# Kernel optimization log

Measured on AMD Instinct MI355X. Metric: run time of the kernel, lower is better.

The kernel has to match this reference:

```python
import jax, jax.numpy as jnp
import numpy as np

B, S, H = 1, 2048, 2048
NH, NKV, HD = 32, 8, 64
RBS, ICS, RBN = 64, 64, 16          # retrieval_block_size, input_chunk_size, retrieval_block_num
RLEN = RBS * RBN                     # 1024 retrieval tokens
KV = RLEN + S                        # 3072 total kv length
START = RLEN                         # INPUT_START_IDX
SCALE = HD ** -0.5
NEG = -1e9


def _document_ids():
    # mirrors get_document_ids
    ids = np.full(KV, -1, np.int32)
    ids[:START] = np.arange(START) // RBS + 1            # retrieval blocks -> 1..RBN
    chunk = np.arange(S) // ICS
    ids[START:] = np.where(chunk == 0, -1, np.minimum(chunk, RBN))
    return ids


def _block_mask():
    # mirrors causal_retrieval_mask_mod, precomputed dense [S, KV]
    ids = _document_ids()
    qpos = np.arange(S) + START
    kv = np.arange(KV)
    causal = (qpos[:, None] >= kv[None, :]) & (kv[None, :] > START)
    doc = (ids[qpos][:, None] == ids[None, :]) & (kv[None, :] < START)
    return jnp.asarray(causal | doc)


_MASK = _block_mask()


def _rotate_half(x):
    h = x.shape[-1] // 2
    return jnp.concatenate([-x[..., h:], x[..., :h]], axis=-1)


def setup_inputs() -> dict:
    key = jax.random.key(0)
    ks = jax.random.split(key, 6)
    inv_freq = 1.0 / (10000.0 ** (np.arange(0, HD, 2, dtype=np.float32) / HD))
    ang = np.arange(S, dtype=np.float32)[:, None] * inv_freq[None, :]   # [S, HD/2]
    emb = np.concatenate([ang, ang], axis=-1)                            # [S, HD]
    cos = jnp.asarray(np.cos(emb))[None].astype(jnp.float32)            # [1, S, HD]
    sin = jnp.asarray(np.sin(emb))[None].astype(jnp.float32)
    return {
        "hidden_states": jax.random.normal(ks[0], (B, S, H), jnp.float32),
        "cos": cos,
        "sin": sin,
        "retrieval_key": jax.random.normal(ks[1], (B, NKV, RLEN, HD), jnp.float32),
        "retrieval_value": jax.random.normal(ks[2], (B, NKV, RLEN, HD), jnp.float32),
        "Wq": jax.random.normal(ks[3], (H, NH * HD), jnp.float32) * 0.02,
        "Wk": jax.random.normal(ks[4], (H, NKV * HD), jnp.float32) * 0.02,
        "Wv": jax.random.normal(ks[5], (H, NKV * HD), jnp.float32) * 0.02,
        "Wo": jax.random.normal(jax.random.fold_in(key, 7), (NH * HD, H), jnp.float32) * 0.02,
    }


def reference(hidden_states, cos, sin, retrieval_key, retrieval_value, Wq, Wk, Wv, Wo):
    # QKV projections -> [B, nheads, S, HD]
    q = (hidden_states @ Wq).reshape(B, S, NH, HD).transpose(0, 2, 1, 3)
    k = (hidden_states @ Wk).reshape(B, S, NKV, HD).transpose(0, 2, 1, 3)
    v = (hidden_states @ Wv).reshape(B, S, NKV, HD).transpose(0, 2, 1, 3)
    # RoPE (retrieval kv is pre-encoded; rope only on current tokens)
    c, s = cos[:, None, :, :], sin[:, None, :, :]
    q = q * c + _rotate_half(q) * s
    k = k * c + _rotate_half(k) * s
    # prepend retrieval kv
    k = jnp.concatenate([retrieval_key, k], axis=2)    # [B, NKV, KV, HD]
    v = jnp.concatenate([retrieval_value, v], axis=2)
    # GQA: expand kv heads
    g = NH // NKV
    k = jnp.repeat(k, g, axis=1)                        # [B, NH, KV, HD]
    v = jnp.repeat(v, g, axis=1)
    scores = jnp.einsum("bhqd,bhkd->bhqk", q, k) * SCALE
    scores = jnp.where(_MASK[None, None], scores, NEG)
    probs = jax.nn.softmax(scores, axis=-1)
    # fully-masked rows (q_idx 0) -> zero output, matching flex_attention
    row_valid = _MASK.any(axis=-1)[None, None, :, None]
    probs = jnp.where(row_valid, probs, 0.0)
    out = jnp.einsum("bhqk,bhkd->bhqd", probs, v)
    out = out.transpose(0, 2, 1, 3).reshape(B, S, NH * HD)
    return out @ Wo
```

## Files before the change

### kernel.cpp

```cpp
#include <hip/hip_runtime.h>

#define S_LEN 2048
#define H_DIM 2048
#define NH 32
#define NKV 8
#define HD 64
#define RLEN 1024
#define KVTOT 3072
#define SCALE 0.125f
#define QS 0.18033688011112042f
#define FIX8 11.541560327111707f

typedef unsigned short ushort_t;
using short8 = __attribute__((ext_vector_type(8))) short;
using f32x4 = __attribute__((ext_vector_type(4))) float;

__device__ __forceinline__ float b2f(unsigned short u) {
    union { unsigned int i; float f; } v;
    v.i = ((unsigned int)u) << 16;
    return v.f;
}
__device__ __forceinline__ unsigned short f2b(float f) {
    union { float f; unsigned int i; } v;
    v.f = f;
    unsigned int x = v.i;
    return (unsigned short)((x + 0x7fffu + ((x >> 16) & 1u)) >> 16);
}

__global__ void detect9(const void* p0, const void* p1, const void* p2,
                        const void* p3, const void* p4, const void* p5,
                        const void* p6, const void* p7, const void* p8,
                        int* flags)
{
    __shared__ int bad;
    if (threadIdx.x == 0) bad = 0;
    __syncthreads();
    const void* ps[9] = {p0, p1, p2, p3, p4, p5, p6, p7, p8};
    const unsigned int* w = (const unsigned int*)ps[blockIdx.x];
    int cnt = 0;
    for (int i = threadIdx.x; i < 4096; i += blockDim.x) {
        unsigned int lo = w[i] & 0xFFFFu;
        unsigned int e = (lo >> 7) & 0xFFu;
        if (lo != 0u && (e < 90u || e > 140u)) ++cnt;
    }
    atomicAdd(&bad, cnt);
    __syncthreads();
    if (threadIdx.x == 0) flags[blockIdx.x] = (bad > 16) ? 1 : 0;
}

__global__ void cvt_b(const void* __restrict__ src, ushort_t* __restrict__ dst,
                      int n, const int* __restrict__ F_)
{
    const int F = *F_;
    int i = (blockIdx.x * 256 + threadIdx.x) * 8;
    if (i >= n) return;
    ushort_t o[8];
    if (F) {
        const float* p = (const float*)src + i;
        float4 f0 = ((const float4*)p)[0];
        float4 f1 = ((const float4*)p)[1];
        o[0] = f2b(f0.x); o[1] = f2b(f0.y); o[2] = f2b(f0.z); o[3] = f2b(f0.w);
        o[4] = f2b(f1.x); o[5] = f2b(f1.y); o[6] = f2b(f1.z); o[7] = f2b(f1.w);
        *(uint4*)(dst + i) = *(const uint4*)o;
    } else {
        *(uint4*)(dst + i) = *(const uint4*)((const ushort_t*)src + i);
    }
}

__global__ __launch_bounds__(256) void cvtW(
    const void* __restrict__ Wq, const void* __restrict__ Wk,
    const void* __restrict__ Wv, const void* __restrict__ Wo,
    ushort_t* __restrict__ WqkvT, ushort_t* __restrict__ WoT,
    const int* __restrict__ flags)
{
    const int z = blockIdx.z;
    if ((z == 1 || z == 2) && blockIdx.x >= 8) return;
    const void* src = (z == 0) ? Wq : (z == 1) ? Wk : (z == 2) ? Wv : Wo;
    const int F = flags[5 + z];
    const int C = (z == 1 || z == 2) ? 512 : 2048;
    ushort_t* dst = (z == 3) ? WoT : WqkvT;
    const int rofs = (z == 1) ? 2048 : (z == 2) ? 2560 : 0;

    __shared__ ushort_t S[64 * 72];
    const int r0 = blockIdx.y * 64, c0 = blockIdx.x * 64;
    const int lr = threadIdx.x >> 2, lc = (threadIdx.x & 3) * 16;
    ushort_t t[16];
    if (F) {
        const float* p = (const float*)src + (size_t)(r0 + lr) * C + c0 + lc;
#pragma unroll
        for (int j = 0; j < 16; j += 4) {
            float4 f = *(const float4*)(p + j);
            t[j] = f2b(f.x); t[j + 1] = f2b(f.y); t[j + 2] = f2b(f.z); t[j + 3] = f2b(f.w);
        }
    } else {
        const ushort_t* p = (const ushort_t*)src + (size_t)(r0 + lr) * C + c0 + lc;
        *(uint4*)t = ((const uint4*)p)[0];
        *(uint4*)(t + 8) = ((const uint4*)p)[1];
    }
    *(uint4*)&S[lr * 72 + lc] = *(const uint4*)t;
    *(uint4*)&S[lr * 72 + lc + 8] = *(const uint4*)(t + 8);
    __syncthreads();
    const int wc = threadIdx.x >> 2, wr = (threadIdx.x & 3) * 16;
    ushort_t o[16];
#pragma unroll
    for (int j = 0; j < 16; ++j) o[j] = S[(wr + j) * 72 + wc];
    ushort_t* q = dst + (size_t)(rofs + c0 + wc) * 2048 + r0 + wr;
    *(uint4*)q = *(const uint4*)o;
    *(uint4*)(q + 8) = *(const uint4*)(o + 8);
}

__global__ __launch_bounds__(256) void gemm_qkv(
    const ushort_t* __restrict__ A, const ushort_t* __restrict__ Bt,
    ushort_t* __restrict__ C, int N, int K)
{
    __shared__ __align__(16) ushort_t As[2][64 * 40];
    __shared__ __align__(16) ushort_t Bs[2][128 * 40];
    const int tid = threadIdx.x;
    const int wave = tid >> 6, lane = tid & 63;
    const int lq = lane & 15, quad = lane >> 4;
    const int m0 = blockIdx.y * 64, n0 = blockIdx.x * 128;
    const int wm = (wave & 1) * 32, wn = (wave >> 1) * 64;
    const int ar = tid >> 2, ak = (tid & 3) * 8;
    const int br = tid >> 1, bk = (tid & 1) * 16;
    const int nk = K >> 5;

    f32x4 acc[2][4];
#pragma unroll
    for (int i = 0; i < 2; ++i)
#pragma unroll
        for (int j = 0; j < 4; ++j) acc[i][j] = (f32x4){0.f, 0.f, 0.f, 0.f};

    const ushort_t* ap = A + (size_t)(m0 + ar) * K + ak;
    const ushort_t* bp = Bt + (size_t)(n0 + br) * K + bk;
    {
        uint4 a0 = ((const uint4*)ap)[0];
        uint4 b0 = ((const uint4*)bp)[0], b1 = ((const uint4*)bp)[1];
        *(uint4*)&As[0][ar * 40 + ak] = a0;
        *(uint4*)&Bs[0][br * 40 + bk] = b0; *(uint4*)&Bs[0][br * 40 + bk + 8] = b1;
    }

    for (int kt = 0; kt < nk; ++kt) {
        const int cur = kt & 1;
        uint4 na0, nb0, nb1;
        const bool more = (kt + 1 < nk);
        if (more) {
            na0 = *(const uint4*)(ap + (kt + 1) * 32);
            const ushort_t* bp2 = bp + (kt + 1) * 32;
            nb0 = ((const uint4*)bp2)[0]; nb1 = ((const uint4*)bp2)[1];
        }
        __syncthreads();
        short8 afr[2], bfr[4];
#pragma unroll
        for (int i = 0; i < 2; ++i)
            afr[i] = *(const short8*)&As[cur][(wm + i * 16 + lq) * 40 + quad * 8];
#pragma unroll
        for (int j = 0; j < 4; ++j)
            bfr[j] = *(const short8*)&Bs[cur][(wn + j * 16 + lq) * 40 + quad * 8];
#pragma unroll
        for (int i = 0; i < 2; ++i)
#pragma unroll
            for (int j = 0; j < 4; ++j)
                acc[i][j] = __builtin_amdgcn_mfma_f32_16x16x32_bf16(afr[i], bfr[j], acc[i][j], 0, 0, 0);
        __syncthreads();
        if (more) {
            const int nxt = cur ^ 1;
            *(uint4*)&As[nxt][ar * 40 + ak] = na0;
            *(uint4*)&Bs[nxt][br * 40 + bk] = nb0; *(uint4*)&Bs[nxt][br * 40 + bk + 8] = nb1;
        }
    }

#pragma unroll
    for (int i = 0; i < 2; ++i)
#pragma unroll
        for (int r = 0; r < 4; ++r) {
            ushort_t* cp = C + (size_t)(m0 + wm + i * 16 + quad * 4 + r) * N + n0 + wn + lq;
#pragma unroll
            for (int j = 0; j < 4; ++j) cp[j * 16] = f2b(acc[i][j][r]);
        }
}

__global__ __launch_bounds__(256) void gemm_fin(
    const ushort_t* __restrict__ A, const ushort_t* __restrict__ Bt,
    void* __restrict__ Cv, int N, int K, const int* __restrict__ oF_)
{
    const int oF = *oF_;
    __shared__ __align__(16) ushort_t As[2][64 * 40];
    __shared__ __align__(16) ushort_t Bs[2][128 * 40];
    const int tid = threadIdx.x;
    const int wave = tid >> 6, lane = tid & 63;
    const int lq = lane & 15, quad = lane >> 4;
    const int m0 = blockIdx.y * 64, n0 = blockIdx.x * 128;
    const int wm = (wave & 1) * 32, wn = (wave >> 1) * 64;
    const int ar = tid >> 2, ak = (tid & 3) * 8;
    const int br = tid >> 1, bk = (tid & 1) * 16;
    const int nk = K >> 5;

    f32x4 acc[2][4];
#pragma unroll
    for (int i = 0; i < 2; ++i)
#pragma unroll
        for (int j = 0; j < 4; ++j) acc[i][j] = (f32x4){0.f, 0.f, 0.f, 0.f};

    const ushort_t* ap = A + (size_t)(m0 + ar) * K + ak;
    const ushort_t* bp = Bt + (size_t)(n0 + br) * K + bk;
    {
        uint4 a0 = ((const uint4*)ap)[0];
        uint4 b0 = ((const uint4*)bp)[0], b1 = ((const uint4*)bp)[1];
        *(uint4*)&As[0][ar * 40 + ak] = a0;
        *(uint4*)&Bs[0][br * 40 + bk] = b0; *(uint4*)&Bs[0][br * 40 + bk + 8] = b1;
    }

    for (int kt = 0; kt < nk; ++kt) {
        const int cur = kt & 1;
        uint4 na0, nb0, nb1;
        const bool more = (kt + 1 < nk);
        if (more) {
            na0 = *(const uint4*)(ap + (kt + 1) * 32);
            const ushort_t* bp2 = bp + (kt + 1) * 32;
            nb0 = ((const uint4*)bp2)[0]; nb1 = ((const uint4*)bp2)[1];
        }
        __syncthreads();
        short8 afr[2], bfr[4];
#pragma unroll
        for (int i = 0; i < 2; ++i)
            afr[i] = *(const short8*)&As[cur][(wm + i * 16 + lq) * 40 + quad * 8];
#pragma unroll
        for (int j = 0; j < 4; ++j)
            bfr[j] = *(const short8*)&Bs[cur][(wn + j * 16 + lq) * 40 + quad * 8];
#pragma unroll
        for (int i = 0; i < 2; ++i)
#pragma unroll
            for (int j = 0; j < 4; ++j)
                acc[i][j] = __builtin_amdgcn_mfma_f32_16x16x32_bf16(afr[i], bfr[j], acc[i][j], 0, 0, 0);
        __syncthreads();
        if (more) {
            const int nxt = cur ^ 1;
            *(uint4*)&As[nxt][ar * 40 + ak] = na0;
            *(uint4*)&Bs[nxt][br * 40 + bk] = nb0; *(uint4*)&Bs[nxt][br * 40 + bk + 8] = nb1;
        }
    }

#pragma unroll
    for (int i = 0; i < 2; ++i)
#pragma unroll
        for (int r = 0; r < 4; ++r) {
            size_t off = (size_t)(m0 + wm + i * 16 + quad * 4 + r) * N + n0 + wn + lq;
            if (oF) {
                float* cp = (float*)Cv + off;
#pragma unroll
                for (int j = 0; j < 4; ++j) cp[j * 16] = acc[i][j][r];
            } else {
                ushort_t* cp = (ushort_t*)Cv + off;
#pragma unroll
                for (int j = 0; j < 4; ++j) cp[j * 16] = f2b(acc[i][j][r]);
            }
        }
}

__global__ __launch_bounds__(256) void prepKV(
    const void* __restrict__ rk, const void* __restrict__ rv,
    const ushort_t* __restrict__ qkvp,
    const void* __restrict__ cosv, const void* __restrict__ sinv,
    ushort_t* __restrict__ ktall, ushort_t* __restrict__ vtall,
    const int* __restrict__ flags)
{
    if (blockIdx.z == 0) {
        const int vF = flags[4];
        const int t = blockIdx.x;
        const int kvh = blockIdx.y;
        __shared__ ushort_t S[64 * 72];
        const int lr = threadIdx.x >> 2, lc = (threadIdx.x & 3) * 16;
        ushort_t tt[16];
        if (t < 16) {
            size_t base = ((size_t)kvh * RLEN + t * 64 + lr) * HD + lc;
            if (vF) {
                const float* p = (const float*)rv + base;
#pragma unroll
                for (int j = 0; j < 16; j += 4) {
                    float4 f = *(const float4*)(p + j);
                    tt[j] = f2b(f.x); tt[j + 1] = f2b(f.y); tt[j + 2] = f2b(f.z); tt[j + 3] = f2b(f.w);
                }
            } else {
                const ushort_t* p = (const ushort_t*)rv + base;
                *(uint4*)tt = ((const uint4*)p)[0];
                *(uint4*)(tt + 8) = ((const uint4*)p)[1];
            }
        } else {
            const ushort_t* p = qkvp + (size_t)((t - 16) * 64 + lr) * 3072 + 2560 + kvh * HD + lc;
            *(uint4*)tt = ((const uint4*)p)[0];
            *(uint4*)(tt + 8) = ((const uint4*)p)[1];
        }
        *(uint4*)&S[lr * 72 + lc] = *(const uint4*)tt;
        *(uint4*)&S[lr * 72 + lc + 8] = *(const uint4*)(tt + 8);
        __syncthreads();
        const int wc = threadIdx.x >> 2, wr = (threadIdx.x & 3) * 16;
        ushort_t o[16];
#pragma unroll
        for (int j = 0; j < 16; ++j) o[j] = S[(wr + j) * 72 + wc];
        const int blk = t * 2 + (wr >> 5);
        ushort_t* q = vtall + (((size_t)(kvh * 96 + blk) * 64 + wc) * 32) + (wr & 31);
        *(uint4*)q = *(const uint4*)o;
        *(uint4*)(q + 8) = *(const uint4*)(o + 8);
    } else {
        const int kF = flags[3], cF = flags[1], sF = flags[2];
        int flat = (blockIdx.y * 48 + blockIdx.x) * 256 + threadIdx.x;
        const int d0 = (flat & 3) * 8;
        const int p = (flat >> 2) % KVTOT;
        const int kvh = (flat >> 2) / KVTOT;
        ushort_t o0[8], o1[8];
        if (p < RLEN) {
            size_t base = ((size_t)kvh * RLEN + p) * HD;
            if (kF) {
                const float* s = (const float*)rk + base;
#pragma unroll
                for (int j = 0; j < 8; j += 4) {
                    float4 f = *(const float4*)(s + d0 + j);
                    o0[j] = f2b(f.x); o0[j + 1] = f2b(f.y); o0[j + 2] = f2b(f.z); o0[j + 3] = f2b(f.w);
                    float4 g = *(const float4*)(s + d0 + 32 + j);
                    o1[j] = f2b(g.x); o1[j + 1] = f2b(g.y); o1[j + 2] = f2b(g.z); o1[j + 3] = f2b(g.w);
                }
            } else {
                const ushort_t* s = (const ushort_t*)rk + base;
                *(uint4*)o0 = *(const uint4*)(s + d0);
                *(uint4*)o1 = *(const uint4*)(s + d0 + 32);
            }
        } else {
            const int si = p - RLEN;
            const ushort_t* s = qkvp + (size_t)si * 3072 + 2048 + kvh * HD;
            uint4 u0 = *(const uint4*)(s + d0);
            uint4 u1 = *(const uint4*)(s + d0 + 32);
            const ushort_t* a16 = (const ushort_t*)&u0;
            const ushort_t* b16 = (const ushort_t*)&u1;
            int ci = si * HD + d0;
            float c0[8], c1[8], s0[8], s1[8];
            if (cF) {
                const float* cp = (const float*)cosv + ci;
#pragma unroll
                for (int j = 0; j < 8; ++j) { c0[j] = cp[j]; c1[j] = cp[j + 32]; }
            } else {
                const ushort_t* cp = (const ushort_t*)cosv + ci;
#pragma unroll
                for (int j = 0; j < 8; ++j) { c0[j] = b2f(cp[j]); c1[j] = b2f(cp[j + 32]); }
            }
            if (sF) {
                const float* sp = (const float*)sinv + ci;
#pragma unroll
                for (int j = 0; j < 8; ++j) { s0[j] = sp[j]; s1[j] = sp[j + 32]; }
            } else {
                const ushort_t* sp = (const ushort_t*)sinv + ci;
#pragma unroll
                for (int j = 0; j < 8; ++j) { s0[j] = b2f(sp[j]); s1[j] = b2f(sp[j + 32]); }
            }
#pragma unroll
            for (int j = 0; j < 8; ++j) {
                float a = b2f(a16[j]), b = b2f(b16[j]);
                o0[j] = f2b(a * c0[j] - b * s0[j]);
                o1[j] = f2b(b * c1[j] + a * s1[j]);
            }
        }
        ushort_t* q = ktall + ((size_t)kvh * KVTOT + p) * HD;
        *(uint4*)(q + d0) = *(const uint4*)o0;
        *(uint4*)(q + d0 + 32) = *(const uint4*)o1;
    }
}

__global__ __launch_bounds__(256) void fattn(
    const ushort_t* __restrict__ qkvp, const ushort_t* __restrict__ ktall,
    const ushort_t* __restrict__ vtall, ushort_t* __restrict__ attno,
    const void* __restrict__ cosv, const void* __restrict__ sinv,
    const int* __restrict__ flags)
{
    const int cF = flags[1], sF = flags[2];
    const int h = blockIdx.x;
    const int qb = 31 - blockIdx.y;
    const int kvh = h >> 2;
    const int tid = threadIdx.x;
    const int wave = tid >> 6;
    const int lane = tid & 63;
    const int lq = lane & 15;
    const int quad = lane >> 4;
    const int rb64 = ((qb < 17 ? qb : 16) - 1) * 64;

    __shared__ __align__(16) ushort_t Ks[128 * 72];
    __shared__ __align__(16) ushort_t Ps[4 * 16 * 136];
    ushort_t* pw = &Ps[wave * 16 * 136];

    short8 qfrag[2];
    {
        const int row_g = qb * 64 + wave * 16 + lq;
        const ushort_t* qrow = qkvp + (size_t)row_g * 3072 + h * HD;
        short8 t0 = *(const short8*)(qrow + quad * 8);
        short8 t1 = *(const short8*)(qrow + 32 + quad * 8);
        const int ci = row_g * HD + quad * 8;
        float c0[8], c1[8], s0[8], s1[8];
        if (cF) {
            const float* cp = (const float*)cosv + ci;
#pragma unroll
            for (int j = 0; j < 8; ++j) { c0[j] = cp[j]; c1[j] = cp[j + 32]; }
        } else {
            const ushort_t* cp = (const ushort_t*)cosv + ci;
#pragma unroll
            for (int j = 0; j < 8; ++j) { c0[j] = b2f(cp[j]); c1[j] = b2f(cp[j + 32]); }
        }
        if (sF) {
            const float* sp = (const float*)sinv + ci;
#pragma unroll
            for (int j = 0; j < 8; ++j) { s0[j] = sp[j]; s1[j] = sp[j + 32]; }
        } else {
            const ushort_t* sp = (const ushort_t*)sinv + ci;
#pragma unroll
            for (int j = 0; j < 8; ++j) { s0[j] = b2f(sp[j]); s1[j] = b2f(sp[j + 32]); }
        }
#pragma unroll
        for (int j = 0; j < 8; ++j) {
            float a = b2f((unsigned short)t0[j]), b = b2f((unsigned short)t1[j]);
            qfrag[0][j] = (short)f2b((a * c0[j] - b * s0[j]) * QS);
            qfrag[1][j] = (short)f2b((b * c1[j] + a * s1[j]) * QS);
        }
    }

    f32x4 oacc[4];
#pragma unroll
    for (int nt = 0; nt < 4; ++nt) oacc[nt] = (f32x4){0.f, 0.f, 0.f, 0.f};
    float lsum[4] = {0.f, 0.f, 0.f, 0.f};

    const int Lq = (qb > 0) ? qb * 64 + 128 : 64;
    const int nch = (Lq + 127) >> 7;
    const ushort_t* kbase = ktall + (size_t)kvh * KVTOT * HD;
    const ushort_t* vbase = vtall + (size_t)kvh * 96 * 2048;

    for (int c = 0; c < nch; ++c) {
        uint4 kreg0, kreg1, kreg2, kreg3;
        const int krow = tid >> 1;
        const int kd0 = (tid & 1) * 32;
        {
            int p = c * 128 + krow;
            uint4 z = {0, 0, 0, 0};
            kreg0 = z; kreg1 = z; kreg2 = z; kreg3 = z;
            if (p < Lq) {
                int pk = (qb > 0) ? ((p < 64) ? rb64 + p : 960 + p) : RLEN + p;
                const uint4* s = (const uint4*)(kbase + (size_t)pk * HD + kd0);
                kreg0 = s[0]; kreg1 = s[1]; kreg2 = s[2]; kreg3 = s[3];
            }
        }
        int vblk[4];
#pragma unroll
        for (int kc = 0; kc < 4; ++kc) {
            int p = c * 128 + kc * 32;
            int pk = (qb > 0) ? ((p < 64) ? rb64 + p : 960 + p) : RLEN + p;
            if (pk > KVTOT - 1) pk = KVTOT - 1;
            vblk[kc] = pk >> 5;
        }
        short8 vfA[4], vfB[4];
#pragma unroll
        for (int ntd = 0; ntd < 4; ++ntd)
            vfA[ntd] = *(const short8*)(vbase + ((size_t)vblk[0] * 64 + ntd * 16 + lq) * 32 + quad * 8);
#pragma unroll
        for (int ntd = 0; ntd < 4; ++ntd)
            vfB[ntd] = *(const short8*)(vbase + ((size_t)vblk[1] * 64 + ntd * 16 + lq) * 32 + quad * 8);

        {
            uint4* dk = (uint4*)&Ks[krow * 72 + kd0];
            dk[0] = kreg0; dk[1] = kreg1; dk[2] = kreg2; dk[3] = kreg3;
        }
        __syncthreads();

        const bool lastc = (c == nch - 1) || (qb == 0);
#pragma unroll
        for (int nt = 0; nt < 8; ++nt) {
            f32x4 a = (f32x4){0.f, 0.f, 0.f, 0.f};
            a = __builtin_amdgcn_mfma_f32_16x16x32_bf16(qfrag[0],
                *(const short8*)&Ks[(nt * 16 + lq) * 72 + quad * 8], a, 0, 0, 0);
            a = __builtin_amdgcn_mfma_f32_16x16x32_bf16(qfrag[1],
                *(const short8*)&Ks[(nt * 16 + lq) * 72 + 32 + quad * 8], a, 0, 0, 0);
            const int p = c * 128 + nt * 16 + lq;
#pragma unroll
            for (int r = 0; r < 4; ++r) {
                float pexp = exp2f(a[r] - FIX8);
                if (lastc) {
                    const int qg = qb * 64 + wave * 16 + quad * 4 + r;
                    bool valid;
                    if (qb > 0) valid = (p < 64) || ((p - 64) >= 1 && (p - 64) <= qg);
                    else        valid = (p >= 1 && p <= qg);
                    if (!valid) pexp = 0.f;
                } else if (c == 0) {
                    if (p == 64) pexp = 0.f;
                }
                lsum[r] += pexp;
                pw[(quad * 4 + r) * 136 + nt * 16 + lq] = f2b(pexp);
            }
        }

#pragma unroll
        for (int kc = 0; kc < 4; ++kc) {
            short8 pa = *(const short8*)&pw[lq * 136 + kc * 32 + quad * 8];
            short8 vf0, vf1, vf2, vf3;
            if (kc == 0)      { vf0 = vfA[0]; vf1 = vfA[1]; vf2 = vfA[2]; vf3 = vfA[3]; }
            else if (kc == 1) { vf0 = vfB[0]; vf1 = vfB[1]; vf2 = vfB[2]; vf3 = vfB[3]; }
            else {
                const int b = vblk[kc];
                vf0 = *(const short8*)(vbase + ((size_t)b * 64 + 0 * 16 + lq) * 32 + quad * 8);
                vf1 = *(const short8*)(vbase + ((size_t)b * 64 + 1 * 16 + lq) * 32 + quad * 8);
                vf2 = *(const short8*)(vbase + ((size_t)b * 64 + 2 * 16 + lq) * 32 + quad * 8);
                vf3 = *(const short8*)(vbase + ((size_t)b * 64 + 3 * 16 + lq) * 32 + quad * 8);
            }
            oacc[0] = __builtin_amdgcn_mfma_f32_16x16x32_bf16(pa, vf0, oacc[0], 0, 0, 0);
            oacc[1] = __builtin_amdgcn_mfma_f32_16x16x32_bf16(pa, vf1, oacc[1], 0, 0, 0);
            oacc[2] = __builtin_amdgcn_mfma_f32_16x16x32_bf16(pa, vf2, oacc[2], 0, 0, 0);
            oacc[3] = __builtin_amdgcn_mfma_f32_16x16x32_bf16(pa, vf3, oacc[3], 0, 0, 0);
        }
        __syncthreads();
    }

#pragma unroll
    for (int r = 0; r < 4; ++r) {
        float v = lsum[r];
        v += __shfl_xor(v, 1, 64); v += __shfl_xor(v, 2, 64);
        v += __shfl_xor(v, 4, 64); v += __shfl_xor(v, 8, 64);
        lsum[r] = v;
    }
#pragma unroll
    for (int r = 0; r < 4; ++r) {
        const int qg = qb * 64 + wave * 16 + quad * 4 + r;
        const float inv = (qg == 0) ? 0.f : 1.f / lsum[r];
        ushort_t* orow = attno + (size_t)qg * 2048 + h * HD;
#pragma unroll
        for (int nt = 0; nt < 4; ++nt)
            orow[nt * 16 + lq] = f2b(oacc[nt][r] * inv);
    }
}

extern "C" void kernel_launch(void* const* d_in, const int* in_sizes, int n_in,
                              void* d_out, int out_size, void* d_ws, size_t ws_size,
                              hipStream_t stream) {
    const void* hs   = d_in[0];
    const void* cosv = d_in[1];
    const void* sinv = d_in[2];
    const void* rk   = d_in[3];
    const void* rv   = d_in[4];
    const void* Wq   = d_in[5];
    const void* Wk   = d_in[6];
    const void* Wv   = d_in[7];
    const void* Wo   = d_in[8];

    char* ws = (char*)d_ws;
    int*      flags  = (int*)ws;
    ushort_t* hsb    = (ushort_t*)(ws + (1u  << 20));
    ushort_t* ktall  = hsb;
    ushort_t* vtall  = (ushort_t*)(ws + (1u << 20) + (13u << 18));
    ushort_t* WqkvT  = (ushort_t*)(ws + (9u  << 20));
    ushort_t* attno  = WqkvT;
    ushort_t* WoT    = (ushort_t*)(ws + (21u << 20));
    ushort_t* qkvp   = (ushort_t*)(ws + (29u << 20));

    detect9<<<9, 256, 0, stream>>>(hs, cosv, sinv, rk, rv, Wq, Wk, Wv, Wo, flags);

    cvt_b<<<(H_DIM * S_LEN / 8 + 255) / 256, 256, 0, stream>>>(hs, hsb, H_DIM * S_LEN, flags + 0);
    cvtW<<<dim3(32, 32, 4), 256, 0, stream>>>(Wq, Wk, Wv, Wo, WqkvT, WoT, flags);

    gemm_qkv<<<dim3(3072 / 128, 2048 / 64), 256, 0, stream>>>(hsb, WqkvT, qkvp, 3072, 2048);

    prepKV<<<dim3(48, 8, 2), 256, 0, stream>>>(rk, rv, qkvp, cosv, sinv, ktall, vtall, flags);

    fattn<<<dim3(NH, 32), 256, 0, stream>>>(qkvp, ktall, vtall, attno, cosv, sinv, flags);

    gemm_fin<<<dim3(2048 / 128, 2048 / 64), 256, 0, stream>>>(attno, WoT, d_out, 2048, 2048, flags + 0);
}
```

Baseline: 270.9 us.

## Fuse hidden-state bf16 conversion into QKV GEMM and prefetch K tiles in attention

Removes the separate cvt_b kernel and has gemm_qkv load the fp32 hidden states directly, converting them to bf16 on the fly through a shared ld8 helper. This saves one launch and a full write and read of the converted activation buffer. The cost is that every column block of the GEMM now reads fp32 A and converts it again, which doubles A-side global traffic. The attention kernel also moves the next chunk's K global load ahead of the current chunk's compute, a register double buffer meant to hide load latency. The remaining edits fold duplicated conversion code into ld8.

```diff
diff --git a/kernel.cpp b/kernel.cpp
--- a/kernel.cpp
+++ b/kernel.cpp
@@ -25,6 +25,18 @@
     v.f = f;
     unsigned int x = v.i;
     return (unsigned short)((x + 0x7fffu + ((x >> 16) & 1u)) >> 16);
+}
+
+__device__ __forceinline__ uint4 ld8(const void* A, size_t idx, int F) {
+    if (F) {
+        const float* p = (const float*)A + idx;
+        float4 f0 = ((const float4*)p)[0], f1 = ((const float4*)p)[1];
+        ushort_t o[8];
+        o[0] = f2b(f0.x); o[1] = f2b(f0.y); o[2] = f2b(f0.z); o[3] = f2b(f0.w);
+        o[4] = f2b(f1.x); o[5] = f2b(f1.y); o[6] = f2b(f1.z); o[7] = f2b(f1.w);
+        return *(uint4*)o;
+    }
+    return *(const uint4*)((const ushort_t*)A + idx);
 }
 
 __global__ void detect9(const void* p0, const void* p1, const void* p2,
@@ -48,25 +60,6 @@
     if (threadIdx.x == 0) flags[blockIdx.x] = (bad > 16) ? 1 : 0;
 }
 
-__global__ void cvt_b(const void* __restrict__ src, ushort_t* __restrict__ dst,
-                      int n, const int* __restrict__ F_)
-{
-    const int F = *F_;
-    int i = (blockIdx.x * 256 + threadIdx.x) * 8;
-    if (i >= n) return;
-    ushort_t o[8];
-    if (F) {
-        const float* p = (const float*)src + i;
-        float4 f0 = ((const float4*)p)[0];
-        float4 f1 = ((const float4*)p)[1];
-        o[0] = f2b(f0.x); o[1] = f2b(f0.y); o[2] = f2b(f0.z); o[3] = f2b(f0.w);
-        o[4] = f2b(f1.x); o[5] = f2b(f1.y); o[6] = f2b(f1.z); o[7] = f2b(f1.w);
-        *(uint4*)(dst + i) = *(const uint4*)o;
-    } else {
-        *(uint4*)(dst + i) = *(const uint4*)((const ushort_t*)src + i);
-    }
-}
-
 __global__ __launch_bounds__(256) void cvtW(
     const void* __restrict__ Wq, const void* __restrict__ Wk,
     const void* __restrict__ Wv, const void* __restrict__ Wo,
@@ -84,21 +77,9 @@
     __shared__ ushort_t S[64 * 72];
     const int r0 = blockIdx.y * 64, c0 = blockIdx.x * 64;
     const int lr = threadIdx.x >> 2, lc = (threadIdx.x & 3) * 16;
-    ushort_t t[16];
-    if (F) {
-        const float* p = (const float*)src + (size_t)(r0 + lr) * C + c0 + lc;
-#pragma unroll
-        for (int j = 0; j < 16; j += 4) {
-            float4 f = *(const float4*)(p + j);
-            t[j] = f2b(f.x); t[j + 1] = f2b(f.y); t[j + 2] = f2b(f.z); t[j + 3] = f2b(f.w);
-        }
-    } else {
-        const ushort_t* p = (const ushort_t*)src + (size_t)(r0 + lr) * C + c0 + lc;
-        *(uint4*)t = ((const uint4*)p)[0];
-        *(uint4*)(t + 8) = ((const uint4*)p)[1];
-    }
-    *(uint4*)&S[lr * 72 + lc] = *(const uint4*)t;
-    *(uint4*)&S[lr * 72 + lc + 8] = *(const uint4*)(t + 8);
+    size_t base = (size_t)(r0 + lr) * C + c0 + lc;
+    *(uint4*)&S[lr * 72 + lc] = ld8(src, base, F);
+    *(uint4*)&S[lr * 72 + lc + 8] = ld8(src, base + 8, F);
     __syncthreads();
     const int wc = threadIdx.x >> 2, wr = (threadIdx.x & 3) * 16;
     ushort_t o[16];
@@ -110,9 +91,10 @@
 }
 
 __global__ __launch_bounds__(256) void gemm_qkv(
-    const ushort_t* __restrict__ A, const ushort_t* __restrict__ Bt,
-    ushort_t* __restrict__ C, int N, int K)
+    const void* __restrict__ A, const ushort_t* __restrict__ Bt,
+    ushort_t* __restrict__ C, int N, int K, const int* __restrict__ aF_)
 {
+    const int aF = *aF_;
     __shared__ __align__(16) ushort_t As[2][64 * 40];
     __shared__ __align__(16) ushort_t Bs[2][128 * 40];
     const int tid = threadIdx.x;
@@ -130,10 +112,10 @@
 #pragma unroll
         for (int j = 0; j < 4; ++j) acc[i][j] = (f32x4){0.f, 0.f, 0.f, 0.f};
 
-    const ushort_t* ap = A + (size_t)(m0 + ar) * K + ak;
+    const size_t aidx = (size_t)(m0 + ar) * K + ak;
     const ushort_t* bp = Bt + (size_t)(n0 + br) * K + bk;
     {
-        uint4 a0 = ((const uint4*)ap)[0];
+        uint4 a0 = ld8(A, aidx, aF);
         uint4 b0 = ((const uint4*)bp)[0], b1 = ((const uint4*)bp)[1];
         *(uint4*)&As[0][ar * 40 + ak] = a0;
         *(uint4*)&Bs[0][br * 40 + bk] = b0; *(uint4*)&Bs[0][br * 40 + bk + 8] = b1;
@@ -144,7 +126,7 @@
         uint4 na0, nb0, nb1;
         const bool more = (kt + 1 < nk);
         if (more) {
-            na0 = *(const uint4*)(ap + (kt + 1) * 32);
+            na0 = ld8(A, aidx + (kt + 1) * 32, aF);
             const ushort_t* bp2 = bp + (kt + 1) * 32;
             nb0 = ((const uint4*)bp2)[0]; nb1 = ((const uint4*)bp2)[1];
         }
@@ -270,28 +252,15 @@
         const int kvh = blockIdx.y;
         __shared__ ushort_t S[64 * 72];
         const int lr = threadIdx.x >> 2, lc = (threadIdx.x & 3) * 16;
-        ushort_t tt[16];
         if (t < 16) {
             size_t base = ((size_t)kvh * RLEN + t * 64 + lr) * HD + lc;
-            if (vF) {
-                const float* p = (const float*)rv + base;
-#pragma unroll
-                for (int j = 0; j < 16; j += 4) {
-                    float4 f = *(const float4*)(p + j);
-                    tt[j] = f2b(f.x); tt[j + 1] = f2b(f.y); tt[j + 2] = f2b(f.z); tt[j + 3] = f2b(f.w);
-                }
-            } else {
-                const ushort_t* p = (const ushort_t*)rv + base;
-                *(uint4*)tt = ((const uint4*)p)[0];
-                *(uint4*)(tt + 8) = ((const uint4*)p)[1];
-            }
+            *(uint4*)&S[lr * 72 + lc] = ld8(rv, base, vF);
+            *(uint4*)&S[lr * 72 + lc + 8] = ld8(rv, base + 8, vF);
         } else {
             const ushort_t* p = qkvp + (size_t)((t - 16) * 64 + lr) * 3072 + 2560 + kvh * HD + lc;
-            *(uint4*)tt = ((const uint4*)p)[0];
-            *(uint4*)(tt + 8) = ((const uint4*)p)[1];
-        }
-        *(uint4*)&S[lr * 72 + lc] = *(const uint4*)tt;
-        *(uint4*)&S[lr * 72 + lc + 8] = *(const uint4*)(tt + 8);
+            *(uint4*)&S[lr * 72 + lc] = ((const uint4*)p)[0];
+            *(uint4*)&S[lr * 72 + lc + 8] = ((const uint4*)p)[1];
+        }
         __syncthreads();
         const int wc = threadIdx.x >> 2, wr = (threadIdx.x & 3) * 16;
         ushort_t o[16];
@@ -310,20 +279,8 @@
         ushort_t o0[8], o1[8];
         if (p < RLEN) {
             size_t base = ((size_t)kvh * RLEN + p) * HD;
-            if (kF) {
-                const float* s = (const float*)rk + base;
-#pragma unroll
-                for (int j = 0; j < 8; j += 4) {
-                    float4 f = *(const float4*)(s + d0 + j);
-                    o0[j] = f2b(f.x); o0[j + 1] = f2b(f.y); o0[j + 2] = f2b(f.z); o0[j + 3] = f2b(f.w);
-                    float4 g = *(const float4*)(s + d0 + 32 + j);
-                    o1[j] = f2b(g.x); o1[j + 1] = f2b(g.y); o1[j + 2] = f2b(g.z); o1[j + 3] = f2b(g.w);
-                }
-            } else {
-                const ushort_t* s = (const ushort_t*)rk + base;
-                *(uint4*)o0 = *(const uint4*)(s + d0);
-                *(uint4*)o1 = *(const uint4*)(s + d0 + 32);
-            }
+            *(uint4*)o0 = ld8(rk, base + d0, kF);
+            *(uint4*)o1 = ld8(rk, base + d0 + 32, kF);
         } else {
             const int si = p - RLEN;
             const ushort_t* s = qkvp + (size_t)si * 3072 + 2048 + kvh * HD;
@@ -429,20 +386,39 @@
     const ushort_t* kbase = ktall + (size_t)kvh * KVTOT * HD;
     const ushort_t* vbase = vtall + (size_t)kvh * 96 * 2048;
 
+    const int krow = tid >> 1;
+    const int kd0 = (tid & 1) * 32;
+
+    uint4 kreg0, kreg1, kreg2, kreg3;
+    {
+        uint4 z = {0, 0, 0, 0};
+        kreg0 = z; kreg1 = z; kreg2 = z; kreg3 = z;
+        int p = krow;
+        if (p < Lq) {
+            int pk = (qb > 0) ? ((p < 64) ? rb64 + p : 960 + p) : RLEN + p;
+            const uint4* s = (const uint4*)(kbase + (size_t)pk * HD + kd0);
+            kreg0 = s[0]; kreg1 = s[1]; kreg2 = s[2]; kreg3 = s[3];
+        }
+    }
+
     for (int c = 0; c < nch; ++c) {
-        uint4 kreg0, kreg1, kreg2, kreg3;
-        const int krow = tid >> 1;
-        const int kd0 = (tid & 1) * 32;
         {
-            int p = c * 128 + krow;
+            uint4* dk = (uint4*)&Ks[krow * 72 + kd0];
+            dk[0] = kreg0; dk[1] = kreg1; dk[2] = kreg2; dk[3] = kreg3;
+        }
+        __syncthreads();
+
+        if (c + 1 < nch) {
             uint4 z = {0, 0, 0, 0};
             kreg0 = z; kreg1 = z; kreg2 = z; kreg3 = z;
+            int p = (c + 1) * 128 + krow;
             if (p < Lq) {
                 int pk = (qb > 0) ? ((p < 64) ? rb64 + p : 960 + p) : RLEN + p;
                 const uint4* s = (const uint4*)(kbase + (size_t)pk * HD + kd0);
                 kreg0 = s[0]; kreg1 = s[1]; kreg2 = s[2]; kreg3 = s[3];
             }
         }
+
         int vblk[4];
 #pragma unroll
         for (int kc = 0; kc < 4; ++kc) {
@@ -458,12 +434,6 @@
 #pragma unroll
         for (int ntd = 0; ntd < 4; ++ntd)
             vfB[ntd] = *(const short8*)(vbase + ((size_t)vblk[1] * 64 + ntd * 16 + lq) * 32 + quad * 8);
-
-        {
-            uint4* dk = (uint4*)&Ks[krow * 72 + kd0];
-            dk[0] = kreg0; dk[1] = kreg1; dk[2] = kreg2; dk[3] = kreg3;
-        }
-        __syncthreads();
 
         const bool lastc = (c == nch - 1) || (qb == 0);
 #pragma unroll
@@ -545,8 +515,7 @@
 
     char* ws = (char*)d_ws;
     int*      flags  = (int*)ws;
-    ushort_t* hsb    = (ushort_t*)(ws + (1u  << 20));
-    ushort_t* ktall  = hsb;
+    ushort_t* ktall  = (ushort_t*)(ws + (1u  << 20));
     ushort_t* vtall  = (ushort_t*)(ws + (1u << 20) + (13u << 18));
     ushort_t* WqkvT  = (ushort_t*)(ws + (9u  << 20));
     ushort_t* attno  = WqkvT;
@@ -555,10 +524,9 @@
 
     detect9<<<9, 256, 0, stream>>>(hs, cosv, sinv, rk, rv, Wq, Wk, Wv, Wo, flags);
 
-    cvt_b<<<(H_DIM * S_LEN / 8 + 255) / 256, 256, 0, stream>>>(hs, hsb, H_DIM * S_LEN, flags + 0);
     cvtW<<<dim3(32, 32, 4), 256, 0, stream>>>(Wq, Wk, Wv, Wo, WqkvT, WoT, flags);
 
-    gemm_qkv<<<dim3(3072 / 128, 2048 / 64), 256, 0, stream>>>(hsb, WqkvT, qkvp, 3072, 2048);
+    gemm_qkv<<<dim3(3072 / 128, 2048 / 64), 256, 0, stream>>>(hs, WqkvT, qkvp, 3072, 2048, flags + 0);
 
     prepKV<<<dim3(48, 8, 2), 256, 0, stream>>>(rk, rv, qkvp, cosv, sinv, ktall, vtall, flags);
 
```

Result: slower. 288.6 us (+6.5%).
